# Performance work log

Hardware: AMD Instinct MI355X
Metric: run time of the kernel (lower is better)

## Reference

```python
import jax, jax.numpy as jnp
import numpy as np
from jax import lax

NUM_CLASS = 3
PRE_MAX = 4096
POST_MAX = 300
IOU_THR = 0.5
SCORE_THR = 0.05
N_ANCHORS = 321408  # 248*216 BEV grid * 6 anchors per location


def setup_inputs() -> dict:
    key = jax.random.key(0)
    k1, k2, k3, k4, k5, k6 = jax.random.split(key, 6)
    box_preds = jax.random.normal(k1, (1, N_ANCHORS, 7), jnp.float32) * 0.3
    cls_preds = jax.random.normal(k2, (1, N_ANCHORS, NUM_CLASS), jnp.float32)
    dir_preds = jax.random.normal(k3, (1, N_ANCHORS, 2), jnp.float32)
    # anchors [x, y, z, w, l, h, r] at realistic KITTI scale
    xy = jax.random.uniform(k4, (1, N_ANCHORS, 2), jnp.float32, 0.0, 70.0)
    z = jnp.full((1, N_ANCHORS, 1), -1.0, jnp.float32)
    wlh = jax.random.uniform(k5, (1, N_ANCHORS, 3), jnp.float32, 0.5, 4.0)
    r = jax.random.uniform(k6, (1, N_ANCHORS, 1), jnp.float32, -np.pi, np.pi)
    anchors = jnp.concatenate([xy, z, wlh, r], axis=-1)
    return {"box_preds": box_preds, "cls_preds": cls_preds,
            "dir_preds": dir_preds, "anchors": anchors}


def decode_boxes(enc, anchors):
    # SECOND box coder decode, code_size = 7
    xa, ya, za, wa, la, ha, ra = jnp.split(anchors, 7, axis=-1)
    xt, yt, zt, wt, lt, ht, rt = jnp.split(enc, 7, axis=-1)
    za = za + ha * 0.5
    diag = jnp.sqrt(la * la + wa * wa)
    xg = xt * diag + xa
    yg = yt * diag + ya
    zg = zt * ha + za
    lg = jnp.exp(lt) * la
    wg = jnp.exp(wt) * wa
    hg = jnp.exp(ht) * ha
    rg = rt + ra
    zg = zg - hg * 0.5
    return jnp.concatenate([xg, yg, zg, wg, lg, hg, rg], axis=-1)


def standup_boxes(b5):
    # b5: [N,5] = (x, y, w, l, r) -> axis-aligned [xmin, ymin, xmax, ymax]
    centers, dims, ang = b5[:, :2], b5[:, 2:4], b5[:, 4]
    signs = jnp.array([[-1., -1.], [-1., 1.], [1., 1.], [1., -1.]], jnp.float32)
    corners = dims[:, None, :] * 0.5 * signs  # [N,4,2]
    c, s = jnp.cos(ang), jnp.sin(ang)
    rot = jnp.stack([jnp.stack([c, -s], -1), jnp.stack([s, c], -1)], axis=-2)  # [N,2,2]
    corners = jnp.einsum('nkj,nji->nki', corners, rot) + centers[:, None, :]
    return jnp.concatenate([corners.min(axis=1), corners.max(axis=1)], axis=-1)


def pairwise_iou(b):
    # b: [N,4] standup boxes
    area = (b[:, 2] - b[:, 0]) * (b[:, 3] - b[:, 1])
    lt = jnp.maximum(b[:, None, :2], b[None, :, :2])
    rb = jnp.minimum(b[:, None, 2:], b[None, :, 2:])
    wh = jnp.clip(rb - lt, 0.0)
    inter = wh[..., 0] * wh[..., 1]
    return inter / (area[:, None] + area[None, :] - inter + 1e-8)


def greedy_nms(iou, valid):
    n = iou.shape[0]
    def body(keep, i):
        suppressed = jnp.any(keep & (iou[i] > IOU_THR))
        ki = valid[i] & (~suppressed)
        return keep.at[i].set(ki), None
    keep, _ = lax.scan(body, jnp.zeros((n,), bool), jnp.arange(n))
    return keep


def reference(box_preds, cls_preds, dir_preds, anchors):
    boxes = decode_boxes(box_preds[0], anchors[0])          # [N,7]
    scores = jax.nn.sigmoid(cls_preds[0])                   # [N,C]
    dir_labels = jnp.argmax(dir_preds[0], axis=-1)          # [N]
    top_scores = scores.max(axis=-1)
    top_labels = jnp.argmax(scores, axis=-1)
    valid = top_scores >= SCORE_THR
    sc = jnp.where(valid, top_scores, -1.0)
    pre_scores, pre_idx = lax.top_k(sc, PRE_MAX)            # sorted desc
    b_nms = standup_boxes(boxes[pre_idx][:, jnp.array([0, 1, 3, 4, 6])])
    iou = pairwise_iou(b_nms)                               # [PRE,PRE]
    keep = greedy_nms(iou, pre_scores > 0.0)
    kept_sc = jnp.where(keep, pre_scores, -1.0)
    post_sc, post_i = lax.top_k(kept_sc, POST_MAX)
    sel = pre_idx[post_i]                                   # original anchor ids
    v = post_sc > 0.0
    sel_boxes = boxes[sel]
    sel_dir = dir_labels[sel]
    opp = (sel_boxes[:, -1] > 0.0) ^ (sel_dir > 0)
    sel_boxes = sel_boxes.at[:, -1].add(
        jnp.where(opp, jnp.float32(np.pi), jnp.float32(0.0)))
    sel_boxes = jnp.where(v[:, None], sel_boxes, 0.0)
    sel_scores = jnp.where(v, post_sc, 0.0)
    sel_labels = jnp.where(v, top_labels[sel], -1)
    return sel_boxes, sel_scores, sel_labels, v
```

## Files before the change

### kernel.cpp

```cpp
#include <hip/hip_runtime.h>

#pragma clang fp contract(off)

#define N_ANCH 321408
#define NQUAD (N_ANCH / 4)
#define KSEL 4096
#define POST 300
#define H1BINS 1024
#define H1BASE 0x3D40u
#define CANDCAP 16384
#define SUPCAP 16
#define WW 256
#define OVFCAP 32

typedef unsigned int u32;
typedef unsigned long long u64;

__device__ __forceinline__ u32 key_of(float m) {
    float s = 1.0f / (1.0f + expf(-m));
    return (s >= 0.05f) ? __float_as_uint(s) : 0u;
}

__global__ __launch_bounds__(1024) void k_keys(const float4* __restrict__ cls4,
                                               uint4* __restrict__ keys4,
                                               u32* __restrict__ hist) {
    __shared__ u32 h0[H1BINS], h1[H1BINS];
    int t = threadIdx.x;
    h0[t] = 0; h1[t] = 0;
    __syncthreads();
    int q = blockIdx.x * 1024 + t;
    if (q < NQUAD) {
        float4 a = cls4[q * 3], b = cls4[q * 3 + 1], d = cls4[q * 3 + 2];
        u32 k0 = key_of(fmaxf(a.x, fmaxf(a.y, a.z)));
        u32 k1 = key_of(fmaxf(a.w, fmaxf(b.x, b.y)));
        u32 k2 = key_of(fmaxf(b.z, fmaxf(b.w, d.x)));
        u32 k3 = key_of(fmaxf(d.y, fmaxf(d.z, d.w)));
        keys4[q] = make_uint4(k0, k1, k2, k3);
        u32* hp = (t & 1) ? h1 : h0;
        atomicAdd(&hp[k0 ? ((k0 >> 16) - H1BASE + 1u) : 0u], 1u);
        atomicAdd(&hp[k1 ? ((k1 >> 16) - H1BASE + 1u) : 0u], 1u);
        atomicAdd(&hp[k2 ? ((k2 >> 16) - H1BASE + 1u) : 0u], 1u);
        atomicAdd(&hp[k3 ? ((k3 >> 16) - H1BASE + 1u) : 0u], 1u);
    }
    __syncthreads();
    u32 c = h0[t] + h1[t];
    if (c) atomicAdd(&hist[t], c);
}

__global__ __launch_bounds__(1024) void k_scan1(const u32* __restrict__ hist, u32* scal) {
    __shared__ u32 sh[1024];
    int t = threadIdx.x;
    int b = 1023 - t;
    u32 s = hist[b];
    sh[t] = s;
    __syncthreads();
    for (int off = 1; off < 1024; off <<= 1) {
        u32 x = sh[t];
        u32 y = (t >= off) ? sh[t - off] : 0u;
        __syncthreads();
        sh[t] = x + y;
        __syncthreads();
    }
    u32 incl = sh[t];
    u32 excl = incl - s;
    if (excl < 4096u && incl >= 4096u) {
        scal[8] = (b > 0) ? (u32)(b - 1) + H1BASE : 0u;
    }
    if (t == 1023) scal[9] = incl - s;
}

__global__ __launch_bounds__(256) void k_compact(const uint4* __restrict__ keys4,
                                                 u32* scal, u64* __restrict__ cand) {
    int q = blockIdx.x * 256 + threadIdx.x;
    bool act = q < NQUAD;
    uint4 kv = act ? keys4[q] : make_uint4(0, 0, 0, 0);
    u32 thr16 = scal[8];
    int lane = threadIdx.x & 63;
    u32 i0 = (u32)q * 4u;
    bool p0 = kv.x && (kv.x >> 16) >= thr16;
    bool p1 = kv.y && (kv.y >> 16) >= thr16;
    bool p2 = kv.z && (kv.z >> 16) >= thr16;
    bool p3 = kv.w && (kv.w >> 16) >= thr16;
    u64 b0 = __ballot(p0), b1 = __ballot(p1), b2 = __ballot(p2), b3 = __ballot(p3);
    u32 n0 = (u32)__popcll(b0), n1 = (u32)__popcll(b1), n2 = (u32)__popcll(b2);
    u32 nw = n0 + n1 + n2 + (u32)__popcll(b3);
    u32 base = 0;
    if (lane == 0 && nw) base = atomicAdd(&scal[5], nw);
    base = (u32)__shfl((int)base, 0);
    u64 lt = (lane == 0) ? 0ull : (~0ull >> (64 - lane));
    if (p0) { u32 p = base + (u32)__popcll(b0 & lt);
              if (p < CANDCAP) cand[p] = (((u64)kv.x) << 32) | (u32)(~(i0 + 0)); }
    if (p1) { u32 p = base + n0 + (u32)__popcll(b1 & lt);
              if (p < CANDCAP) cand[p] = (((u64)kv.y) << 32) | (u32)(~(i0 + 1)); }
    if (p2) { u32 p = base + n0 + n1 + (u32)__popcll(b2 & lt);
              if (p < CANDCAP) cand[p] = (((u64)kv.z) << 32) | (u32)(~(i0 + 2)); }
    if (p3) { u32 p = base + n0 + n1 + n2 + (u32)__popcll(b3 & lt);
              if (p < CANDCAP) cand[p] = (((u64)kv.w) << 32) | (u32)(~(i0 + 3)); }
}

__global__ __launch_bounds__(256) void k_rankpart(const u32* __restrict__ scal,
                                                  const u64* __restrict__ cand,
                                                  u32* __restrict__ rank) {
    __shared__ u64 ch[512];
    u32 nc = scal[5]; if (nc > CANDCAP) nc = CANDCAP;
    u32 cb = blockIdx.x * 256u;
    u32 jb = blockIdx.y * 512u;
    if (cb >= nc || jb >= nc) return;
    u32 t = threadIdx.x;
    for (u32 j = t; j < 512u; j += 256u)
        ch[j] = (jb + j < nc) ? cand[jb + j] : 0ull;
    __syncthreads();
    u32 me = cb + t;
    u64 mine = (me < nc) ? cand[me] : ~0ull;
    u32 r = 0;
    #pragma unroll 8
    for (int j = 0; j < 512; ++j) r += (ch[j] > mine) ? 1u : 0u;
    if (me < nc && r) atomicAdd(&rank[me], r);
}

__global__ void k_scatter(const u32* __restrict__ scal, const u64* __restrict__ cand,
                          const u32* __restrict__ rank, u64* __restrict__ sorted) {
    u32 nc = scal[5]; if (nc > CANDCAP) nc = CANDCAP;
    u32 t = blockIdx.x * 256u + threadIdx.x;
    if (t < nc) {
        u32 r = rank[t];
        if (r < (u32)KSEL) sorted[r] = cand[t];
    }
}

__device__ __forceinline__ void decode_box(u64 cpack, const float* __restrict__ boxp,
                                           const float* __restrict__ anch, float b[7]) {
    u32 key = (u32)(cpack >> 32);
    u32 idx = ~((u32)(cpack & 0xFFFFFFFFull));
    if (key == 0u) idx = 0u;
    const float* a7 = anch + (size_t)idx * 7;
    const float* t7 = boxp + (size_t)idx * 7;
    float xa = a7[0], ya = a7[1], za = a7[2], wa = a7[3], la = a7[4], ha = a7[5], ra = a7[6];
    float xt = t7[0], yt = t7[1], zt = t7[2], wt = t7[3], lt_ = t7[4], ht = t7[5], rt = t7[6];
    za = za + ha * 0.5f;
    float diag = sqrtf(la * la + wa * wa);
    float xg = xt * diag + xa;
    float yg = yt * diag + ya;
    float zg = zt * ha + za;
    float lg = expf(lt_) * la;
    float wg = expf(wt) * wa;
    float hg = expf(ht) * ha;
    float rg = rt + ra;
    zg = zg - hg * 0.5f;
    b[0] = xg; b[1] = yg; b[2] = zg; b[3] = wg; b[4] = lg; b[5] = hg; b[6] = rg;
}

__device__ __forceinline__ float4 standup_box(const float b[7], float* areao) {
    float xg = b[0], yg = b[1], wg = b[3], lg = b[4], rg = b[6];
    float cc = cosf(rg), ss = sinf(rg);
    float dx = wg * 0.5f, dy = lg * 0.5f;
    const float sxs[4] = {-1.f, -1.f, 1.f, 1.f};
    const float sys[4] = {-1.f, 1.f, 1.f, -1.f};
    float minx = 1e30f, miny = 1e30f, maxx = -1e30f, maxy = -1e30f;
    #pragma unroll
    for (int k = 0; k < 4; ++k) {
        float cx = dx * sxs[k], cy = dy * sys[k];
        float px = cx * cc + cy * ss;
        float py = cx * (-ss) + cy * cc;
        px = px + xg; py = py + yg;
        minx = fminf(minx, px); maxx = fmaxf(maxx, px);
        miny = fminf(miny, py); maxy = fmaxf(maxy, py);
    }
    *areao = (maxx - minx) * (maxy - miny);
    return make_float4(minx, miny, maxx, maxy);
}

__global__ void k_decode(const u64* __restrict__ sel2, const float* __restrict__ boxp,
                         const float* __restrict__ anch, float4* __restrict__ bb,
                         float* __restrict__ area) {
    int r = blockIdx.x * blockDim.x + threadIdx.x;
    if (r >= KSEL) return;
    float b[7];
    decode_box(sel2[r], boxp, anch, b);
    float a;
    bb[r] = standup_box(b, &a);
    area[r] = a;
}

__global__ __launch_bounds__(64) void k_mask(const float4* __restrict__ bb,
                                             const float* __restrict__ area,
                                             u64* __restrict__ mask,
                                             u32* __restrict__ sup_cnt,
                                             u32* __restrict__ sup_ent) {
    int t = threadIdx.x;
    int rb = blockIdx.y, cb = blockIdx.x;
    int i = rb * 64 + t;
    if (cb < rb) { mask[(size_t)i * 64 + cb] = 0ull; return; }
    __shared__ float4 ob[64];
    __shared__ float oa[64];
    int jg0 = cb * 64;
    ob[t] = bb[jg0 + t];
    oa[t] = area[jg0 + t];
    __syncthreads();
    float4 m4 = bb[i];
    float ma = area[i];
    u64 bits = 0;
    for (int j = 0; j < 64; ++j) {
        int jg = jg0 + j;
        if (jg == i) continue;
        float4 o = ob[j];
        float ltx = fmaxf(m4.x, o.x), lty = fmaxf(m4.y, o.y);
        float rbx = fminf(m4.z, o.z), rby = fminf(m4.w, o.w);
        float w = fmaxf(rbx - ltx, 0.0f), h = fmaxf(rby - lty, 0.0f);
        float inter = w * h;
        float iou = inter / (ma + oa[j] - inter + 1e-8f);
        if (iou > 0.5f) bits |= (1ULL << j);
    }
    mask[(size_t)i * 64 + cb] = bits;
    u64 bset = bits;
    while (bset) {
        int j = (int)__builtin_ctzll(bset);
        bset &= bset - 1;
        int jg = jg0 + j;
        if (jg > i) {
            u32 p = atomicAdd(&sup_cnt[i], 1u);
            if (p < SUPCAP) sup_ent[(size_t)i * SUPCAP + p] = (u32)jg;
        }
    }
}

__global__ __launch_bounds__(256, 1) void k_serial(const u64* __restrict__ mask,
                                                   const u32* __restrict__ sup_cnt,
                                                   const u32* __restrict__ sup_ent,
                                                   u32* __restrict__ keep_list,
                                                   u32* __restrict__ scal) {
    int t = threadIdx.x;
    int lane = t & 63;
    int wave = t >> 6;
    __shared__ u64 ls_avail[64];
    __shared__ u32 ls_excl[64];
    __shared__ int ls_cand[WW];
    __shared__ u64 ls_m[WW][4];
    __shared__ u64 ls_wv[4];
    __shared__ u64 ls_unc[4];
    __shared__ u32 ls_ovf[OVFCAP];
    __shared__ u32 ls_novf;

    if (t < 64) {
        u32 nvt = scal[9];
        u32 nv = (nvt < (u32)KSEL) ? nvt : (u32)KSEL;
        int lo = t * 64;
        u64 a;
        if ((int)nv >= lo + 64) a = ~0ull;
        else if ((int)nv <= lo) a = 0ull;
        else a = (((u64)1) << (nv - lo)) - 1ull;
        ls_avail[t] = a;
    }
    __syncthreads();

    int cnt = 0;
    for (;;) {
        ls_m[t][0] = 0; ls_m[t][1] = 0; ls_m[t][2] = 0; ls_m[t][3] = 0;
        ls_cand[t] = -1;
        if (t == 0) ls_novf = 0;
        __syncthreads();
        if (t < 64) {
            u64 avail = ls_avail[t];
            u32 pc = (u32)__popcll(avail);
            u32 pre = pc;
            #pragma unroll
            for (int off = 1; off < 64; off <<= 1) {
                u32 y = __shfl_up(pre, (unsigned)off);
                if (lane >= off) pre += y;
            }
            u32 excl = pre - pc;
            ls_excl[t] = excl;
            if (pc && excl < (u32)WW) {
                u64 a = avail;
                u32 o = excl;
                while (a && o < (u32)WW) {
                    int b = (int)__builtin_ctzll(a);
                    a &= a - 1;
                    ls_cand[o++] = t * 64 + b;
                }
            }
        }
        __syncthreads();
        int cj = ls_cand[t];
        bool valid = cj >= 0;
        {
            u64 wvb = __ballot(valid);
            if (lane == 0) ls_wv[wave] = wvb;
        }
        if (ls_cand[0] < 0) break;
        int cs = valid ? cj : 0;
        const uint4* ep = (const uint4*)(sup_ent + (size_t)cs * SUPCAP);
        uint4 e0 = ep[0], e1 = ep[1], e2 = ep[2], e3 = ep[3];
        u32 scnt = sup_cnt[cs];
        if (!valid) scnt = 0;
        u32 ecap = (scnt < (u32)SUPCAP) ? scnt : (u32)SUPCAP;
        u32 ent[SUPCAP] = {e0.x, e0.y, e0.z, e0.w, e1.x, e1.y, e1.z, e1.w,
                           e2.x, e2.y, e2.z, e2.w, e3.x, e3.y, e3.z, e3.w};
        bool ovf = valid && (scnt > (u32)SUPCAP);
        #pragma unroll
        for (int e = 0; e < SUPCAP; ++e) {
            u32 r = ent[e];
            if ((u32)e < ecap && r < (u32)KSEL) {
                u64 aw = ls_avail[r >> 6];
                if ((aw >> (r & 63)) & 1ull) {
                    u64 below = (r & 63) ? (aw & ((1ull << (r & 63)) - 1ull)) : 0ull;
                    u32 slot = ls_excl[r >> 6] + (u32)__popcll(below);
                    if (slot < (u32)WW)
                        atomicOr(&ls_m[slot][t >> 6], 1ull << (t & 63));
                }
            }
        }
        if (ovf) { u32 p = atomicAdd(&ls_novf, 1u); if (p < OVFCAP) ls_ovf[p] = (u32)t; }
        __syncthreads();
        u32 novf = ls_novf; if (novf > OVFCAP) novf = OVFCAP;
        for (u32 oi = 0; oi < novf; ++oi) {
            int s = (int)ls_ovf[oi];
            int ci = ls_cand[s];
            if (t < 64) {
                u64 w = mask[(size_t)ci * 64 + t] & ls_avail[t];
                while (w) {
                    int b = (int)__builtin_ctzll(w);
                    w &= w - 1;
                    u64 aw = ls_avail[t];
                    u64 below = b ? (aw & ((1ull << b) - 1ull)) : 0ull;
                    u32 slot = ls_excl[t] + (u32)__popcll(below);
                    if (slot < (u32)WW && slot != (u32)s)
                        atomicOr(&ls_m[slot][s >> 6], 1ull << (s & 63));
                }
            }
        }
        __syncthreads();
        u64 my0 = ls_m[t][0], my1 = ls_m[t][1], my2 = ls_m[t][2], my3 = ls_m[t][3];
        bool unc = valid && ((my0 | my1 | my2 | my3) != 0ull);
        {
            u64 ub = __ballot(unc);
            if (lane == 0) ls_unc[wave] = ub;
        }
        __syncthreads();
        u64 wv0 = ls_wv[0], wv1 = ls_wv[1], wv2 = ls_wv[2], wv3 = ls_wv[3];
        u64 u0 = ls_unc[0], u1 = ls_unc[1], u2 = ls_unc[2], u3 = ls_unc[3];
        u64 c0 = wv0 & ~u0, c1 = wv1 & ~u1, c2 = wv2 & ~u2, c3 = wv3 & ~u3;
        #pragma unroll
        for (int blk = 0; blk < 4; ++blk) {
            u64 uw = (blk == 0) ? u0 : (blk == 1) ? u1 : (blk == 2) ? u2 : u3;
            while (uw) {
                int j2 = (int)__builtin_ctzll(uw);
                uw &= uw - 1;
                int j = blk * 64 + j2;
                u64 m0 = ls_m[j][0], m1 = ls_m[j][1], m2 = ls_m[j][2], m3 = ls_m[j][3];
                u64 sup = (m0 & c0) | (m1 & c1) | (m2 & c2) | (m3 & c3);
                if (!sup) {
                    if (blk == 0) c0 |= 1ull << j2;
                    else if (blk == 1) c1 |= 1ull << j2;
                    else if (blk == 2) c2 |= 1ull << j2;
                    else c3 |= 1ull << j2;
                }
            }
        }
        u64 myc = (t < 64) ? c0 : (t < 128) ? c1 : (t < 192) ? c2 : c3;
        bool amC = valid && ((myc >> (t & 63)) & 1ull);
        {
            u32 rk = 0;
            if (wave > 0) rk += (u32)__popcll(c0);
            if (wave > 1) rk += (u32)__popcll(c1);
            if (wave > 2) rk += (u32)__popcll(c2);
            u64 below = (t & 63) ? (myc & ((1ull << (t & 63)) - 1ull)) : 0ull;
            rk += (u32)__popcll(below);
            if (amC && cnt + (int)rk < POST) keep_list[cnt + rk] = (u32)cj;
        }
        int tot = (int)(__popcll(c0) + __popcll(c1) + __popcll(c2) + __popcll(c3));
        if (cnt + tot >= POST) { cnt = POST; break; }
        cnt += tot;
        if (amC) {
            #pragma unroll
            for (int e = 0; e < SUPCAP; ++e) {
                u32 r = ent[e];
                if ((u32)e < ecap && r < (u32)KSEL)
                    atomicAnd(&ls_avail[r >> 6], ~(1ull << (r & 63)));
            }
            atomicAnd(&ls_avail[cj >> 6], ~(1ull << (cj & 63)));
        }
        for (u32 oi = 0; oi < novf; ++oi) {
            int s = (int)ls_ovf[oi];
            u64 sc = (s < 64) ? c0 : (s < 128) ? c1 : (s < 192) ? c2 : c3;
            if ((sc >> (s & 63)) & 1ull) {
                int ci = ls_cand[s];
                if (t < 64) {
                    u64 w = mask[(size_t)ci * 64 + t];
                    if (w) atomicAnd(&ls_avail[t], ~w);
                }
            }
        }
        __syncthreads();
    }
    if (t == 0) scal[7] = (u32)(cnt < POST ? cnt : POST);
}

__global__ void k_final(const u32* __restrict__ scal, const u32* __restrict__ keep_list,
                        const u64* __restrict__ sel2, const float* __restrict__ boxp,
                        const float* __restrict__ anch, const float* __restrict__ cls,
                        const float* __restrict__ dirp, float* __restrict__ out) {
    int t = blockIdx.x * blockDim.x + threadIdx.x;
    if (t >= POST) return;
    u32 m = scal[7];
    float* ob = out;
    float* os = out + POST * 7;
    float* ol = os + POST;
    float* ov = ol + POST;
    if (t < (int)m) {
        u32 r = keep_list[t];
        u64 cp = sel2[r];
        u32 key = (u32)(cp >> 32);
        u32 i = ~((u32)(cp & 0xFFFFFFFFull));
        float b[7];
        decode_box(cp, boxp, anch, b);
        float d0 = dirp[(size_t)i * 2], d1 = dirp[(size_t)i * 2 + 1];
        int dl = (d1 > d0) ? 1 : 0;
        int pos = (b[6] > 0.0f) ? 1 : 0;
        if (pos ^ dl) b[6] = b[6] + 3.14159265358979323846f;
        for (int q = 0; q < 7; ++q) ob[(size_t)t * 7 + q] = b[q];
        os[t] = __uint_as_float(key);
        float s0 = 1.0f / (1.0f + expf(-cls[(size_t)i * 3]));
        float s1 = 1.0f / (1.0f + expf(-cls[(size_t)i * 3 + 1]));
        float s2 = 1.0f / (1.0f + expf(-cls[(size_t)i * 3 + 2]));
        int lab = 0; float best = s0;
        if (s1 > best) { lab = 1; best = s1; }
        if (s2 > best) { lab = 2; }
        ol[t] = (float)lab;
        ov[t] = 1.0f;
    } else {
        for (int q = 0; q < 7; ++q) ob[(size_t)t * 7 + q] = 0.0f;
        os[t] = 0.0f;
        ol[t] = -1.0f;
        ov[t] = 0.0f;
    }
}

extern "C" void kernel_launch(void* const* d_in, const int* in_sizes, int n_in,
                              void* d_out, int out_size, void* d_ws, size_t ws_size,
                              hipStream_t stream) {
    const float* box_preds = (const float*)d_in[0];
    const float* cls_preds = (const float*)d_in[1];
    const float* dir_preds = (const float*)d_in[2];
    const float* anchors   = (const float*)d_in[3];
    float* out = (float*)d_out;

    unsigned char* w = (unsigned char*)d_ws;
    size_t off = 0;
    auto nxt = [&](size_t bytes) -> void* {
        void* p = (void*)(w + off);
        off = (off + bytes + 255) & ~(size_t)255;
        return p;
    };
    u32* hist1     = (u32*)nxt(H1BINS * 4);
    u32* scal      = (u32*)nxt(64 * 4);
    u64* sel2      = (u64*)nxt((size_t)KSEL * 8);
    u32* rank      = (u32*)nxt((size_t)CANDCAP * 4);
    u32* sup_cnt   = (u32*)nxt((size_t)KSEL * 4);
    u64* cand      = (u64*)nxt((size_t)CANDCAP * 8);
    u64* mask      = (u64*)nxt((size_t)KSEL * 64 * 8);
    u32* sup_ent   = (u32*)nxt((size_t)KSEL * SUPCAP * 4);
    u32* keep_list = (u32*)nxt(512 * 4);
    float4* bb     = (float4*)nxt((size_t)KSEL * 16);
    float* area    = (float*)nxt((size_t)KSEL * 4);
    u32* keys      = (u32*)nxt((size_t)N_ANCH * 4);

    hipMemsetAsync(hist1, 0,
                   (size_t)H1BINS * 4 + 256 + (size_t)KSEL * 8 + (size_t)CANDCAP * 4
                   + (size_t)KSEL * 4,
                   stream);

    k_keys<<<(NQUAD + 1023) / 1024, 1024, 0, stream>>>((const float4*)cls_preds,
                                                       (uint4*)keys, hist1);
    k_scan1<<<1, 1024, 0, stream>>>(hist1, scal);
    k_compact<<<(NQUAD + 255) / 256, 256, 0, stream>>>((const uint4*)keys, scal, cand);
    dim3 rg(CANDCAP / 256, CANDCAP / 512);
    k_rankpart<<<rg, 256, 0, stream>>>(scal, cand, rank);
    k_scatter<<<CANDCAP / 256, 256, 0, stream>>>(scal, cand, rank, sel2);
    k_decode<<<KSEL / 256, 256, 0, stream>>>(sel2, box_preds, anchors, bb, area);
    dim3 mg(64, 64);
    k_mask<<<mg, 64, 0, stream>>>(bb, area, mask, sup_cnt, sup_ent);
    k_serial<<<1, 256, 0, stream>>>(mask, sup_cnt, sup_ent, keep_list, scal);
    k_final<<<2, 256, 0, stream>>>(scal, keep_list, sel2, box_preds, anchors, cls_preds, dir_preds, out);
}
```

Baseline: 86.07 us.

## Fuse rank, scatter and decode kernels; drop memset via in-kernel zeroing and per-block histograms

The separate rank, scatter and decode kernels become one kernel. The last block to finish each candidate column, detected with a completion counter, scatters its ranked candidates and decodes their boxes directly. The memset is removed: k_keys zeroes the scalar, sel2, rank, sup_cnt and counter region itself and writes per-block histograms, which k_scan1 then sums instead of relying on global atomics. The aim is fewer launches and less launch overhead. In exchange the scan does more serial reads, and correctness now depends on the last-block fence pattern and on the zeroed region lining up exactly with the workspace layout.

```diff
diff --git a/kernel.cpp b/kernel.cpp
--- a/kernel.cpp
+++ b/kernel.cpp
@@ -4,6 +4,7 @@
 
 #define N_ANCH 321408
 #define NQUAD (N_ANCH / 4)
+#define NKB 79
 #define KSEL 4096
 #define POST 300
 #define H1BINS 1024
@@ -12,6 +13,8 @@
 #define SUPCAP 16
 #define WW 256
 #define OVFCAP 32
+#define ZERO_BYTES (256 + 32768 + 65536 + 16384 + 256)
+#define ZERO_U4 (ZERO_BYTES / 16)
 
 typedef unsigned int u32;
 typedef unsigned long long u64;
@@ -23,19 +26,21 @@
 
 __global__ __launch_bounds__(1024) void k_keys(const float4* __restrict__ cls4,
                                                uint4* __restrict__ keys4,
-                                               u32* __restrict__ hist) {
+                                               u32* __restrict__ hist_part,
+                                               uint4* __restrict__ zbase) {
     __shared__ u32 h0[H1BINS], h1[H1BINS];
     int t = threadIdx.x;
     h0[t] = 0; h1[t] = 0;
     __syncthreads();
-    int q = blockIdx.x * 1024 + t;
-    if (q < NQUAD) {
-        float4 a = cls4[q * 3], b = cls4[q * 3 + 1], d = cls4[q * 3 + 2];
+    int g = blockIdx.x * 1024 + t;
+    if (g < ZERO_U4) zbase[g] = make_uint4(0, 0, 0, 0);
+    if (g < NQUAD) {
+        float4 a = cls4[g * 3], b = cls4[g * 3 + 1], d = cls4[g * 3 + 2];
         u32 k0 = key_of(fmaxf(a.x, fmaxf(a.y, a.z)));
         u32 k1 = key_of(fmaxf(a.w, fmaxf(b.x, b.y)));
         u32 k2 = key_of(fmaxf(b.z, fmaxf(b.w, d.x)));
         u32 k3 = key_of(fmaxf(d.y, fmaxf(d.z, d.w)));
-        keys4[q] = make_uint4(k0, k1, k2, k3);
+        keys4[g] = make_uint4(k0, k1, k2, k3);
         u32* hp = (t & 1) ? h1 : h0;
         atomicAdd(&hp[k0 ? ((k0 >> 16) - H1BASE + 1u) : 0u], 1u);
         atomicAdd(&hp[k1 ? ((k1 >> 16) - H1BASE + 1u) : 0u], 1u);
@@ -43,15 +48,16 @@
         atomicAdd(&hp[k3 ? ((k3 >> 16) - H1BASE + 1u) : 0u], 1u);
     }
     __syncthreads();
-    u32 c = h0[t] + h1[t];
-    if (c) atomicAdd(&hist[t], c);
-}
-
-__global__ __launch_bounds__(1024) void k_scan1(const u32* __restrict__ hist, u32* scal) {
+    hist_part[blockIdx.x * H1BINS + t] = h0[t] + h1[t];
+}
+
+__global__ __launch_bounds__(1024) void k_scan1(const u32* __restrict__ hist_part,
+                                                u32* scal) {
     __shared__ u32 sh[1024];
     int t = threadIdx.x;
     int b = 1023 - t;
-    u32 s = hist[b];
+    u32 s = 0;
+    for (int r = 0; r < NKB; ++r) s += hist_part[r * H1BINS + b];
     sh[t] = s;
     __syncthreads();
     for (int off = 1; off < 1024; off <<= 1) {
@@ -98,36 +104,6 @@
               if (p < CANDCAP) cand[p] = (((u64)kv.w) << 32) | (u32)(~(i0 + 3)); }
 }
 
-__global__ __launch_bounds__(256) void k_rankpart(const u32* __restrict__ scal,
-                                                  const u64* __restrict__ cand,
-                                                  u32* __restrict__ rank) {
-    __shared__ u64 ch[512];
-    u32 nc = scal[5]; if (nc > CANDCAP) nc = CANDCAP;
-    u32 cb = blockIdx.x * 256u;
-    u32 jb = blockIdx.y * 512u;
-    if (cb >= nc || jb >= nc) return;
-    u32 t = threadIdx.x;
-    for (u32 j = t; j < 512u; j += 256u)
-        ch[j] = (jb + j < nc) ? cand[jb + j] : 0ull;
-    __syncthreads();
-    u32 me = cb + t;
-    u64 mine = (me < nc) ? cand[me] : ~0ull;
-    u32 r = 0;
-    #pragma unroll 8
-    for (int j = 0; j < 512; ++j) r += (ch[j] > mine) ? 1u : 0u;
-    if (me < nc && r) atomicAdd(&rank[me], r);
-}
-
-__global__ void k_scatter(const u32* __restrict__ scal, const u64* __restrict__ cand,
-                          const u32* __restrict__ rank, u64* __restrict__ sorted) {
-    u32 nc = scal[5]; if (nc > CANDCAP) nc = CANDCAP;
-    u32 t = blockIdx.x * 256u + threadIdx.x;
-    if (t < nc) {
-        u32 r = rank[t];
-        if (r < (u32)KSEL) sorted[r] = cand[t];
-    }
-}
-
 __device__ __forceinline__ void decode_box(u64 cpack, const float* __restrict__ boxp,
                                            const float* __restrict__ anch, float b[7]) {
     u32 key = (u32)(cpack >> 32);
@@ -170,16 +146,50 @@
     return make_float4(minx, miny, maxx, maxy);
 }
 
-__global__ void k_decode(const u64* __restrict__ sel2, const float* __restrict__ boxp,
-                         const float* __restrict__ anch, float4* __restrict__ bb,
-                         float* __restrict__ area) {
-    int r = blockIdx.x * blockDim.x + threadIdx.x;
-    if (r >= KSEL) return;
-    float b[7];
-    decode_box(sel2[r], boxp, anch, b);
-    float a;
-    bb[r] = standup_box(b, &a);
-    area[r] = a;
+__global__ __launch_bounds__(256) void k_rankfuse(const u32* __restrict__ scal,
+                                                  const u64* __restrict__ cand,
+                                                  u32* __restrict__ rank,
+                                                  u32* __restrict__ dcnt,
+                                                  const float* __restrict__ boxp,
+                                                  const float* __restrict__ anch,
+                                                  u64* __restrict__ sel2,
+                                                  float4* __restrict__ bb,
+                                                  float* __restrict__ area) {
+    __shared__ u64 ch[512];
+    __shared__ u32 lastv;
+    u32 nc = scal[5]; if (nc > CANDCAP) nc = CANDCAP;
+    u32 cb = blockIdx.x * 256u;
+    u32 jb = blockIdx.y * 512u;
+    if (cb >= nc) return;
+    u32 t = threadIdx.x;
+    if (jb < nc) {
+        for (u32 j = t; j < 512u; j += 256u)
+            ch[j] = (jb + j < nc) ? cand[jb + j] : 0ull;
+        __syncthreads();
+        u32 me = cb + t;
+        u64 mine = (me < nc) ? cand[me] : ~0ull;
+        u32 r = 0;
+        #pragma unroll 8
+        for (int j = 0; j < 512; ++j) r += (ch[j] > mine) ? 1u : 0u;
+        if (me < nc && r) atomicAdd(&rank[me], r);
+    }
+    __threadfence();
+    if (t == 0) lastv = atomicAdd(&dcnt[blockIdx.x], 1u);
+    __syncthreads();
+    if (lastv != gridDim.y - 1) return;
+    u32 me = cb + t;
+    if (me < nc) {
+        u32 r = atomicAdd(&rank[me], 0u);
+        if (r < (u32)KSEL) {
+            u64 cp = cand[me];
+            sel2[r] = cp;
+            float bx[7];
+            decode_box(cp, boxp, anch, bx);
+            float a;
+            bb[r] = standup_box(bx, &a);
+            area[r] = a;
+        }
+    }
 }
 
 __global__ __launch_bounds__(64) void k_mask(const float4* __restrict__ bb,
@@ -452,11 +462,12 @@
         off = (off + bytes + 255) & ~(size_t)255;
         return p;
     };
-    u32* hist1     = (u32*)nxt(H1BINS * 4);
     u32* scal      = (u32*)nxt(64 * 4);
     u64* sel2      = (u64*)nxt((size_t)KSEL * 8);
     u32* rank      = (u32*)nxt((size_t)CANDCAP * 4);
     u32* sup_cnt   = (u32*)nxt((size_t)KSEL * 4);
+    u32* dcnt      = (u32*)nxt(64 * 4);
+    u32* hist_part = (u32*)nxt((size_t)NKB * H1BINS * 4);
     u64* cand      = (u64*)nxt((size_t)CANDCAP * 8);
     u64* mask      = (u64*)nxt((size_t)KSEL * 64 * 8);
     u32* sup_ent   = (u32*)nxt((size_t)KSEL * SUPCAP * 4);
@@ -465,19 +476,13 @@
     float* area    = (float*)nxt((size_t)KSEL * 4);
     u32* keys      = (u32*)nxt((size_t)N_ANCH * 4);
 
-    hipMemsetAsync(hist1, 0,
-                   (size_t)H1BINS * 4 + 256 + (size_t)KSEL * 8 + (size_t)CANDCAP * 4
-                   + (size_t)KSEL * 4,
-                   stream);
-
-    k_keys<<<(NQUAD + 1023) / 1024, 1024, 0, stream>>>((const float4*)cls_preds,
-                                                       (uint4*)keys, hist1);
-    k_scan1<<<1, 1024, 0, stream>>>(hist1, scal);
+    k_keys<<<NKB, 1024, 0, stream>>>((const float4*)cls_preds, (uint4*)keys,
+                                     hist_part, (uint4*)scal);
+    k_scan1<<<1, 1024, 0, stream>>>(hist_part, scal);
     k_compact<<<(NQUAD + 255) / 256, 256, 0, stream>>>((const uint4*)keys, scal, cand);
     dim3 rg(CANDCAP / 256, CANDCAP / 512);
-    k_rankpart<<<rg, 256, 0, stream>>>(scal, cand, rank);
-    k_scatter<<<CANDCAP / 256, 256, 0, stream>>>(scal, cand, rank, sel2);
-    k_decode<<<KSEL / 256, 256, 0, stream>>>(sel2, box_preds, anchors, bb, area);
+    k_rankfuse<<<rg, 256, 0, stream>>>(scal, cand, rank, dcnt, box_preds, anchors,
+                                       sel2, bb, area);
     dim3 mg(64, 64);
     k_mask<<<mg, 64, 0, stream>>>(bb, area, mask, sup_cnt, sup_ent);
     k_serial<<<1, 256, 0, stream>>>(mask, sup_cnt, sup_ent, keep_list, scal);
```

New measurement: 123.9 us. 1.44x slower.
